# Kernel optimization log

Measured on AMD Instinct MI355X. Metric: run time of the kernel, lower is better.

The kernel has to match this reference:

```python
import jax, jax.numpy as jnp
import numpy as np

N = 50000          # nodes
E = 800000         # edges (before self-loops)
IN = 128           # in_dim
HID = 128          # hidden_dim
HEADS = 4
G = 256            # graphs in batch
EPS = 1e-5         # batchnorm eps
NEG_SLOPE = 0.2    # GATConv leaky_relu slope


def _gat_layer(x, src, dst, W, a_src, a_dst, bias, H, C, concat):
    """PyG-style GATConv (self-loops already appended to src/dst)."""
    n = x.shape[0]
    h = (x @ W).reshape(n, H, C)                       # [N,H,C]
    s_src = (h * a_src).sum(-1)                        # [N,H]
    s_dst = (h * a_dst).sum(-1)                        # [N,H]
    e = jax.nn.leaky_relu(s_src[src] + s_dst[dst], NEG_SLOPE)   # [E',H]
    m = jax.ops.segment_max(e, dst, num_segments=n)    # segment-wise softmax
    ex = jnp.exp(e - m[dst])
    den = jax.ops.segment_sum(ex, dst, num_segments=n)
    alpha = ex / den[dst]                              # [E',H]
    out = jax.ops.segment_sum(alpha[..., None] * h[src], dst, num_segments=n)  # [N,H,C]
    out = out.reshape(n, H * C) if concat else out.mean(axis=1)
    return out + bias


def _bn(x, gamma, beta):
    # PyG BatchNorm over nodes (training-mode batch statistics)
    mu = x.mean(axis=0)
    var = x.var(axis=0)
    return gamma * (x - mu) * jax.lax.rsqrt(var + EPS) + beta


def setup_inputs() -> dict:
    key = jax.random.key(0)
    ks = jax.random.split(key, 32)
    d = {}
    d["x"] = jax.random.normal(ks[0], (N, IN), dtype=jnp.float32)
    d["edge_index"] = jax.random.randint(ks[1], (2, E), 0, N, dtype=jnp.int64)
    d["batch_idx"] = jnp.sort(jax.random.randint(ks[2], (N,), 0, G, dtype=jnp.int64))
    dims = [(IN, HEADS, HID, True), (HID * HEADS, HEADS, HID, True), (HID * HEADS, 1, HID, False)]
    for i, (din, H, C, concat) in enumerate(dims):
        d[f"W{i}"] = jax.random.normal(ks[3 + 4 * i], (din, H * C), dtype=jnp.float32) * 0.05
        d[f"att_src{i}"] = jax.random.normal(ks[4 + 4 * i], (H, C), dtype=jnp.float32) * 0.05
        d[f"att_dst{i}"] = jax.random.normal(ks[5 + 4 * i], (H, C), dtype=jnp.float32) * 0.05
        out_w = H * C if concat else C
        d[f"bias{i}"] = jnp.zeros((out_w,), dtype=jnp.float32)
        d[f"gamma{i}"] = jnp.ones((out_w,), dtype=jnp.float32)
        d[f"beta{i}"] = jnp.zeros((out_w,), dtype=jnp.float32)
    return d


def reference(x, edge_index, batch_idx,
              W0, att_src0, att_dst0, bias0, gamma0, beta0,
              W1, att_src1, att_dst1, bias1, gamma1, beta1,
              W2, att_src2, att_dst2, bias2, gamma2, beta2):
    n = x.shape[0]
    loops = jnp.arange(n, dtype=edge_index.dtype)
    src = jnp.concatenate([edge_index[0], loops])
    dst = jnp.concatenate([edge_index[1], loops])
    layers = [
        (W0, att_src0, att_dst0, bias0, gamma0, beta0, HEADS, HID, True),
        (W1, att_src1, att_dst1, bias1, gamma1, beta1, HEADS, HID, True),
        (W2, att_src2, att_dst2, bias2, gamma2, beta2, 1, HID, False),
    ]
    h = x
    for (W, a_s, a_d, b, g, bt, H, C, concat) in layers:
        h = _gat_layer(h, src, dst, W, a_s, a_d, b, H, C, concat)
        h = jax.nn.elu(_bn(h, g, bt))
        # dropout: identity in eval mode
    # global_mean_pool over batch_idx
    sums = jax.ops.segment_sum(h, batch_idx, num_segments=G)
    cnt = jax.ops.segment_sum(jnp.ones((n,), dtype=h.dtype), batch_idx, num_segments=G)
    return sums / jnp.maximum(cnt, 1.0)[:, None]
```

## Files before the change

### kernel.cpp

```cpp
#include <hip/hip_runtime.h>
#include <math.h>
#include <stdint.h>

#define N_NODES 50000
#define N_EDGES 800000
#define EP      (N_EDGES + N_NODES)
#define G_GRAPHS 256
#define BN_EPS   1e-5f
#define NEG_SLOPE 0.2f

typedef short short8 __attribute__((ext_vector_type(8)));
typedef float f32x4 __attribute__((ext_vector_type(4)));
typedef unsigned short u16;

static __device__ __forceinline__ float lrelu(float x) {
    return x > 0.f ? x : NEG_SLOPE * x;
}

static __device__ __forceinline__ u16 bf16hi(float f) {
    unsigned u = __float_as_uint(f);
    u += 0x7FFFu + ((u >> 16) & 1u);
    return (u16)(u >> 16);
}
static __device__ __forceinline__ float bf2f(u16 h) {
    return __uint_as_float((unsigned)h << 16);
}

static __device__ __forceinline__ void gld_lds16(const void* g, void* l) {
    __builtin_amdgcn_global_load_lds((const __attribute__((address_space(1))) void*)g,
                                     (__attribute__((address_space(3))) void*)l, 16, 0, 0);
}

static __device__ __forceinline__ float2 h2f2(unsigned u) {
    union { unsigned u; _Float16 h[2]; } c;
    c.u = u;
    return make_float2((float)c.h[0], (float)c.h[1]);
}

__global__ void k_hist(const int* __restrict__ ei, int* __restrict__ deg) {
    int stride = gridDim.x * blockDim.x;
    for (int e = blockIdx.x * blockDim.x + threadIdx.x; e < EP; e += stride) {
        int d = (e < N_EDGES) ? ei[N_EDGES + e] : (e - N_EDGES);
        atomicAdd(&deg[d], 1);
    }
}

__global__ void k_scan1(const int* __restrict__ deg, int* __restrict__ row_start,
                        int* __restrict__ totals) {
    __shared__ int buf[1024];
    int t = threadIdx.x;
    int i = blockIdx.x * 1024 + t;
    int v = (i < N_NODES) ? deg[i] : 0;
    buf[t] = v;
    __syncthreads();
    for (int off = 1; off < 1024; off <<= 1) {
        int add = (t >= off) ? buf[t - off] : 0;
        __syncthreads();
        buf[t] += add;
        __syncthreads();
    }
    if (i < N_NODES) row_start[i] = buf[t] - v;
    if (t == 1023) totals[blockIdx.x] = buf[t];
}

__global__ void k_scan2(int* __restrict__ totals, int nb) {
    if (threadIdx.x == 0 && blockIdx.x == 0) {
        int run = 0;
        for (int i = 0; i < nb; ++i) { int v = totals[i]; totals[i] = run; run += v; }
    }
}

__global__ void k_scan3(int* __restrict__ row_start, const int* __restrict__ totals) {
    int i = blockIdx.x * blockDim.x + threadIdx.x;
    if (i < N_NODES) row_start[i] += totals[i >> 10];
    if (i == 0) row_start[N_NODES] = EP;
}

__global__ void k_scatter(const int* __restrict__ ei, const int* __restrict__ row_start,
                          int* __restrict__ cursor, int* __restrict__ csr_src) {
    int stride = gridDim.x * blockDim.x;
    for (int e = blockIdx.x * blockDim.x + threadIdx.x; e < EP; e += stride) {
        int s, d;
        if (e < N_EDGES) { s = ei[e]; d = ei[N_EDGES + e]; }
        else             { s = d = e - N_EDGES; }
        int pos = row_start[d] + atomicAdd(&cursor[d], 1);
        csr_src[pos] = s;
    }
}

__global__ void k_cvtW(const float* __restrict__ W, u16* __restrict__ bthi,
                       u16* __restrict__ btlo, int Nc, int nsh, int KS) {
    int i = blockIdx.x * 256 + threadIdx.x;
    if (i >= (KS << 5) * Nc) return;
    int k = i >> nsh;
    int n = i & (Nc - 1);
    int c = n >> 7, col = n & 127;
    int ks = k >> 5, kq = (k >> 3) & 3, j = k & 7;
    size_t idx = ((size_t)(c * KS + ks)) * 4096 + kq * 1024 + col * 8 + j;
    float v = W[i];
    u16 h = bf16hi(v);
    bthi[idx] = h;
    btlo[idx] = bf16hi(v - bf2f(h));
}

__global__ void k_bnprep(const float* __restrict__ bnsum, const float* __restrict__ bnsq,
                         const float* __restrict__ gamma, const float* __restrict__ beta,
                         float* __restrict__ scale, float* __restrict__ shift, int W) {
    int f = blockIdx.x * 256 + threadIdx.x;
    if (f >= W) return;
    const float invN = 1.f / (float)N_NODES;
    float mean = bnsum[f] * invN;
    float var  = bnsq[f] * invN - mean * mean;
    float sc = gamma[f] * rsqrtf(var + BN_EPS);
    scale[f] = sc;
    shift[f] = beta[f] - mean * sc;
}

template<int AMODE>
__launch_bounds__(256)
__global__ void k_gemm_mfma(const void* __restrict__ Av, const u16* __restrict__ bthi,
                            const u16* __restrict__ btlo, _Float16* __restrict__ C2,
                            float* __restrict__ sSg, float* __restrict__ sDg,
                            const float* __restrict__ asr, const float* __restrict__ adr,
                            const float* __restrict__ scale, const float* __restrict__ shift,
                            int M, int K, int Nc) {
    __shared__ u16 Ah[4096], Al[4096], Bh[4096], Bl[4096];
    __shared__ float rS[128], rD[128];
    const int t    = threadIdx.x;
    const int lane = t & 63, wv = t >> 6;
    const int wr = wv >> 1, wc = wv & 1;
    const int lr = lane & 15, kq = lane >> 4;
    const int r0 = blockIdx.x * 128, c0 = blockIdx.y * 128;
    const int KS = K >> 5;
    const int H = Nc >> 7;
    const int head = blockIdx.y;

    const int ar = t >> 1;
    const int ahf = t & 1;
    const int garow = r0 + ar;
    const bool avalid = garow < M;
    const float*    arowF = (const float*)Av + (size_t)garow * K + ahf * 16;
    const _Float16* arowH = (const _Float16*)Av + (size_t)garow * K + ahf * 16;

    const size_t bchunk0 = (size_t)blockIdx.y * KS * 4096;

    f32x4 acc[4][4];
    #pragma unroll
    for (int m = 0; m < 4; ++m)
        #pragma unroll
        for (int n = 0; n < 4; ++n) {
            acc[m][n][0] = 0.f; acc[m][n][1] = 0.f;
            acc[m][n][2] = 0.f; acc[m][n][3] = 0.f;
        }

    for (int ks = 0; ks < KS; ++ks) {
        float f[16];
        float4 av[4];
        uint4 u0, u1;
        if constexpr (AMODE == 0) {
            const float4* ap = (const float4*)(arowF + ks * 32);
            if (avalid) { av[0] = ap[0]; av[1] = ap[1]; av[2] = ap[2]; av[3] = ap[3]; }
            else av[0] = av[1] = av[2] = av[3] = make_float4(0.f, 0.f, 0.f, 0.f);
        } else {
            if (avalid) {
                u0 = *(const uint4*)(arowH + ks * 32);
                u1 = *(const uint4*)(arowH + ks * 32 + 8);
            } else {
                u0.x = u0.y = u0.z = u0.w = 0u;
                u1.x = u1.y = u1.z = u1.w = 0u;
            }
        }
        __syncthreads();

        if constexpr (AMODE == 0) {
            f[0]=av[0].x; f[1]=av[0].y; f[2]=av[0].z; f[3]=av[0].w;
            f[4]=av[1].x; f[5]=av[1].y; f[6]=av[1].z; f[7]=av[1].w;
            f[8]=av[2].x; f[9]=av[2].y; f[10]=av[2].z; f[11]=av[2].w;
            f[12]=av[3].x; f[13]=av[3].y; f[14]=av[3].z; f[15]=av[3].w;
        } else {
            float2 p0 = h2f2(u0.x), p1 = h2f2(u0.y), p2 = h2f2(u0.z), p3 = h2f2(u0.w);
            float2 p4 = h2f2(u1.x), p5 = h2f2(u1.y), p6 = h2f2(u1.z), p7 = h2f2(u1.w);
            f[0]=p0.x; f[1]=p0.y; f[2]=p1.x; f[3]=p1.y;
            f[4]=p2.x; f[5]=p2.y; f[6]=p3.x; f[7]=p3.y;
            f[8]=p4.x; f[9]=p4.y; f[10]=p5.x; f[11]=p5.y;
            f[12]=p6.x; f[13]=p6.y; f[14]=p7.x; f[15]=p7.y;
            const float* scp = scale + ks * 32 + ahf * 16;
            const float* shp = shift + ks * 32 + ahf * 16;
            #pragma unroll
            for (int i = 0; i < 4; ++i) {
                float4 sc = *(const float4*)(scp + 4 * i);
                float4 sh = *(const float4*)(shp + 4 * i);
                float y;
                y = fmaf(f[4*i+0], sc.x, sh.x); f[4*i+0] = y > 0.f ? y : expm1f(y);
                y = fmaf(f[4*i+1], sc.y, sh.y); f[4*i+1] = y > 0.f ? y : expm1f(y);
                y = fmaf(f[4*i+2], sc.z, sh.z); f[4*i+2] = y > 0.f ? y : expm1f(y);
                y = fmaf(f[4*i+3], sc.w, sh.w); f[4*i+3] = y > 0.f ? y : expm1f(y);
            }
        }

        u16 hi[16], lo[16];
        #pragma unroll
        for (int i = 0; i < 16; ++i) {
            hi[i] = bf16hi(f[i]);
            lo[i] = bf16hi(f[i] - bf2f(hi[i]));
        }
        #pragma unroll
        for (int q = 0; q < 2; ++q) {
            int kqi = ahf * 2 + q;
            int off = kqi * 1024 + ar * 8;
            int4 wh, wl;
            wh.x = (unsigned)hi[q*8+0] | ((unsigned)hi[q*8+1] << 16);
            wh.y = (unsigned)hi[q*8+2] | ((unsigned)hi[q*8+3] << 16);
            wh.z = (unsigned)hi[q*8+4] | ((unsigned)hi[q*8+5] << 16);
            wh.w = (unsigned)hi[q*8+6] | ((unsigned)hi[q*8+7] << 16);
            wl.x = (unsigned)lo[q*8+0] | ((unsigned)lo[q*8+1] << 16);
            wl.y = (unsigned)lo[q*8+2] | ((unsigned)lo[q*8+3] << 16);
            wl.z = (unsigned)lo[q*8+4] | ((unsigned)lo[q*8+5] << 16);
            wl.w = (unsigned)lo[q*8+6] | ((unsigned)lo[q*8+7] << 16);
            *(int4*)&Ah[off] = wh;
            *(int4*)&Al[off] = wl;
        }

        const u16* bhs = bthi + bchunk0 + (size_t)ks * 4096;
        const u16* bls = btlo + bchunk0 + (size_t)ks * 4096;
        #pragma unroll
        for (int p = 0; p < 2; ++p) {
            int ge = p * 2048 + wv * 512 + lane * 8;
            int le = p * 2048 + wv * 512;
            gld_lds16(bhs + ge, &Bh[le]);
            gld_lds16(bls + ge, &Bl[le]);
        }
        __syncthreads();

        short8 afh[4], afl[4], bfh[4], bfl[4];
        #pragma unroll
        for (int m = 0; m < 4; ++m) {
            int row = wr * 64 + m * 16 + lr;
            int off = kq * 1024 + row * 8;
            afh[m] = *(const short8*)&Ah[off];
            afl[m] = *(const short8*)&Al[off];
        }
        #pragma unroll
        for (int n = 0; n < 4; ++n) {
            int col = wc * 64 + n * 16 + lr;
            int off = kq * 1024 + col * 8;
            bfh[n] = *(const short8*)&Bh[off];
            bfl[n] = *(const short8*)&Bl[off];
        }
        #pragma unroll
        for (int m = 0; m < 4; ++m)
            #pragma unroll
            for (int n = 0; n < 4; ++n) {
                acc[m][n] = __builtin_amdgcn_mfma_f32_16x16x32_bf16(afh[m], bfh[n], acc[m][n], 0, 0, 0);
                acc[m][n] = __builtin_amdgcn_mfma_f32_16x16x32_bf16(afh[m], bfl[n], acc[m][n], 0, 0, 0);
                acc[m][n] = __builtin_amdgcn_mfma_f32_16x16x32_bf16(afl[m], bfh[n], acc[m][n], 0, 0, 0);
            }
    }

    float aS[4], aD[4];
    #pragma unroll
    for (int n = 0; n < 4; ++n) {
        int c = c0 + wc * 64 + n * 16 + lr;
        aS[n] = asr[c];
        aD[n] = adr[c];
    }
    __syncthreads();
    if (t < 128) { rS[t] = 0.f; rD[t] = 0.f; }
    __syncthreads();
    #pragma unroll
    for (int m = 0; m < 4; ++m) {
        #pragma unroll
        for (int j = 0; j < 4; ++j) {
            float ps = 0.f, pd = 0.f;
            #pragma unroll
            for (int n = 0; n < 4; ++n) {
                float v = acc[m][n][j];
                ps += v * aS[n];
                pd += v * aD[n];
            }
            #pragma unroll
            for (int off = 1; off < 16; off <<= 1) {
                ps += __shfl_xor(ps, off, 64);
                pd += __shfl_xor(pd, off, 64);
            }
            if (lr == 0) {
                int row = wr * 64 + m * 16 + kq * 4 + j;
                atomicAdd(&rS[row], ps);
                atomicAdd(&rD[row], pd);
            }
        }
    }
    __syncthreads();
    if (t < 128) {
        int r = r0 + t;
        if (r < M) {
            sSg[(size_t)r * H + head] = rS[t];
            sDg[(size_t)r * H + head] = rD[t];
        }
    }

    #pragma unroll
    for (int m = 0; m < 4; ++m) {
        int rowb = r0 + wr * 64 + m * 16 + kq * 4;
        #pragma unroll
        for (int n = 0; n < 4; ++n) {
            int col = c0 + wc * 64 + n * 16 + lr;
            #pragma unroll
            for (int j = 0; j < 4; ++j) {
                int r = rowb + j;
                if (r < M) C2[(size_t)r * Nc + col] = (_Float16)acc[m][n][j];
            }
        }
    }
}

template<int H>
__global__ void k_attn(const float* __restrict__ s_src, const float* __restrict__ s_dst,
                       const int* __restrict__ row_start, const int* __restrict__ csr,
                       float* __restrict__ alpha) {
    int n = blockIdx.x;
    int lane = threadIdx.x;
    const int EPI = 64 / H;
    int head = lane % H;
    int eo   = lane / H;
    int lo = row_start[n], hi = row_start[n + 1];
    float sd = s_dst[n * H + head];
    float* al = alpha + (size_t)head * EP;

    float mx = -INFINITY;
    for (int p = lo + eo; p < hi; p += EPI) {
        int s = csr[p];
        float e = lrelu(s_src[s * H + head] + sd);
        al[p] = e;
        mx = fmaxf(mx, e);
    }
    #pragma unroll
    for (int off = H; off < 64; off <<= 1) mx = fmaxf(mx, __shfl_xor(mx, off, 64));

    float sum = 0.f;
    for (int p = lo + eo; p < hi; p += EPI) {
        float ex = expf(al[p] - mx);
        al[p] = ex;
        sum += ex;
    }
    #pragma unroll
    for (int off = H; off < 64; off <<= 1) sum += __shfl_xor(sum, off, 64);

    float inv = 1.f / sum;
    for (int p = lo + eo; p < hi; p += EPI) al[p] *= inv;
}

template<int H, int CPT>
__global__ void k_agg2(const _Float16* __restrict__ hb2, const float* __restrict__ alpha,
                       const int* __restrict__ row_start, const int* __restrict__ csr,
                       const float* __restrict__ bias, _Float16* __restrict__ out) {
    const int W = H * 128;
    int n = blockIdx.x;
    int t = threadIdx.x;
    int c0 = t * CPT;
    int head = c0 >> 7;
    const float* al = alpha + (size_t)head * EP;
    int lo = row_start[n], hi = row_start[n + 1];
    float acc[CPT];
    #pragma unroll
    for (int j = 0; j < CPT; ++j) acc[j] = 0.f;

    int p = lo;
    for (; p + 4 <= hi; p += 4) {
        int s0 = csr[p], s1 = csr[p+1], s2 = csr[p+2], s3 = csr[p+3];
        float l0 = al[p], l1 = al[p+1], l2 = al[p+2], l3 = al[p+3];
        if constexpr (CPT == 4) {
            uint2 v0 = *(const uint2*)&hb2[(size_t)s0 * W + c0];
            uint2 v1 = *(const uint2*)&hb2[(size_t)s1 * W + c0];
            uint2 v2 = *(const uint2*)&hb2[(size_t)s2 * W + c0];
            uint2 v3 = *(const uint2*)&hb2[(size_t)s3 * W + c0];
            float2 a, b;
            a = h2f2(v0.x); b = h2f2(v0.y);
            acc[0] += l0*a.x; acc[1] += l0*a.y; acc[2] += l0*b.x; acc[3] += l0*b.y;
            a = h2f2(v1.x); b = h2f2(v1.y);
            acc[0] += l1*a.x; acc[1] += l1*a.y; acc[2] += l1*b.x; acc[3] += l1*b.y;
            a = h2f2(v2.x); b = h2f2(v2.y);
            acc[0] += l2*a.x; acc[1] += l2*a.y; acc[2] += l2*b.x; acc[3] += l2*b.y;
            a = h2f2(v3.x); b = h2f2(v3.y);
            acc[0] += l3*a.x; acc[1] += l3*a.y; acc[2] += l3*b.x; acc[3] += l3*b.y;
        } else {
            unsigned v0 = *(const unsigned*)&hb2[(size_t)s0 * W + c0];
            unsigned v1 = *(const unsigned*)&hb2[(size_t)s1 * W + c0];
            unsigned v2 = *(const unsigned*)&hb2[(size_t)s2 * W + c0];
            unsigned v3 = *(const unsigned*)&hb2[(size_t)s3 * W + c0];
            float2 a;
            a = h2f2(v0); acc[0] += l0*a.x; acc[1] += l0*a.y;
            a = h2f2(v1); acc[0] += l1*a.x; acc[1] += l1*a.y;
            a = h2f2(v2); acc[0] += l2*a.x; acc[1] += l2*a.y;
            a = h2f2(v3); acc[0] += l3*a.x; acc[1] += l3*a.y;
        }
    }
    for (; p < hi; ++p) {
        int s0 = csr[p];
        float l0 = al[p];
        if constexpr (CPT == 4) {
            uint2 v0 = *(const uint2*)&hb2[(size_t)s0 * W + c0];
            float2 a = h2f2(v0.x), b = h2f2(v0.y);
            acc[0] += l0*a.x; acc[1] += l0*a.y; acc[2] += l0*b.x; acc[3] += l0*b.y;
        } else {
            float2 a = h2f2(*(const unsigned*)&hb2[(size_t)s0 * W + c0]);
            acc[0] += l0*a.x; acc[1] += l0*a.y;
        }
    }

    union { _Float16 h[CPT]; unsigned u[CPT/2]; } pk;
    #pragma unroll
    for (int j = 0; j < CPT; ++j) pk.h[j] = (_Float16)(acc[j] + bias[c0 + j]);
    if constexpr (CPT == 4)
        *(uint2*)&out[(size_t)n * W + c0] = *(uint2*)pk.u;
    else
        *(unsigned*)&out[(size_t)n * W + c0] = pk.u[0];
}

__global__ void k_bnstat2(const _Float16* __restrict__ x, float* __restrict__ bnsum,
                          float* __restrict__ bnsq, int W) {
    const int RPB = 64;
    int t  = threadIdx.x;
    int r0 = blockIdx.x * RPB;
    int r1 = min(r0 + RPB, N_NODES);
    float s0 = 0.f, q0 = 0.f, s1 = 0.f, q1 = 0.f;
    for (int r = r0; r < r1; ++r) {
        float2 v = h2f2(*(const unsigned*)&x[(size_t)r * W + 2 * t]);
        s0 += v.x; q0 += v.x * v.x;
        s1 += v.y; q1 += v.y * v.y;
    }
    atomicAdd(&bnsum[2*t],   s0);
    atomicAdd(&bnsq[2*t],    q0);
    atomicAdd(&bnsum[2*t+1], s1);
    atomicAdd(&bnsq[2*t+1],  q1);
}

__global__ void k_pool(const _Float16* __restrict__ x, const int* __restrict__ batch,
                       const float* __restrict__ scale, const float* __restrict__ shift,
                       float* __restrict__ out) {
    int g = blockIdx.x;
    int f = threadIdx.x;
    int a = 0, b = N_NODES;
    while (a < b) { int m = (a + b) >> 1; if (batch[m] < g) a = m + 1; else b = m; }
    int lo = a;
    b = N_NODES;
    while (a < b) { int m = (a + b) >> 1; if (batch[m] < g + 1) a = m + 1; else b = m; }
    int hi = a;
    float sc = scale[f], sh = shift[f];
    float s = 0.f;
    for (int r = lo; r < hi; ++r) {
        float v = (float)x[(size_t)r * 128 + f];
        float y = fmaf(v, sc, sh);
        s += (y > 0.f) ? y : expm1f(y);
    }
    int cnt = hi - lo;
    out[g * 128 + f] = s / (float)(cnt > 0 ? cnt : 1);
}

extern "C" void kernel_launch(void* const* d_in, const int* in_sizes, int n_in,
                              void* d_out, int out_size, void* d_ws, size_t ws_size,
                              hipStream_t stream) {
    const float* x     = (const float*)d_in[0];
    const int*   ei    = (const int*)d_in[1];
    const int*   batch = (const int*)d_in[2];
    const float* Wm[3]  = {(const float*)d_in[3],  (const float*)d_in[9],  (const float*)d_in[15]};
    const float* asr[3] = {(const float*)d_in[4],  (const float*)d_in[10], (const float*)d_in[16]};
    const float* adr[3] = {(const float*)d_in[5],  (const float*)d_in[11], (const float*)d_in[17]};
    const float* bia[3] = {(const float*)d_in[6],  (const float*)d_in[12], (const float*)d_in[18]};
    const float* gam[3] = {(const float*)d_in[7],  (const float*)d_in[13], (const float*)d_in[19]};
    const float* bet[3] = {(const float*)d_in[8],  (const float*)d_in[14], (const float*)d_in[20]};

    char* w = (char*)d_ws;
    auto alloc = [&](size_t bytes) -> void* {
        void* p = (void*)w;
        w += (bytes + 255) & ~(size_t)255;
        return p;
    };
    _Float16* act2   = (_Float16*)alloc((size_t)N_NODES * 512 * 2);
    _Float16* act128 = (_Float16*)alloc((size_t)N_NODES * 128 * 2);
    _Float16* hb2    = (_Float16*)alloc((size_t)N_NODES * 512 * 2);
    float*   alpha = (float*)alloc((size_t)EP * 4 * 4);
    int* csr_src   = (int*)alloc((size_t)EP * 4);
    int* row_start = (int*)alloc((size_t)(N_NODES + 1) * 4);
    int* deg       = (int*)alloc((size_t)N_NODES * 4);
    int* cursor    = (int*)alloc((size_t)N_NODES * 4);
    float* s_src = (float*)alloc((size_t)N_NODES * 4 * 4);
    float* s_dst = (float*)alloc((size_t)N_NODES * 4 * 4);
    float* bn    = (float*)alloc(1024 * 4);
    float* scl   = (float*)alloc(512 * 4);
    float* shf   = (float*)alloc(512 * 4);
    int* totals  = (int*)alloc(64 * 4);
    u16* bthi = (u16*)alloc((size_t)512 * 512 * 2);
    u16* btlo = (u16*)alloc((size_t)512 * 512 * 2);

    hipMemsetAsync(deg, 0, (size_t)N_NODES * 4, stream);
    hipMemsetAsync(cursor, 0, (size_t)N_NODES * 4, stream);
    k_hist<<<512, 256, 0, stream>>>(ei, deg);
    k_scan1<<<(N_NODES + 1023) / 1024, 1024, 0, stream>>>(deg, row_start, totals);
    k_scan2<<<1, 64, 0, stream>>>(totals, (N_NODES + 1023) / 1024);
    k_scan3<<<(N_NODES + 255) / 256, 256, 0, stream>>>(row_start, totals);
    k_scatter<<<512, 256, 0, stream>>>(ei, row_start, cursor, csr_src);

    auto layer = [&](const void* Ain, int K, int li, int H, int amode, _Float16* outAct) {
        int Wd = H * 128;
        int nsh = (Wd == 512) ? 9 : 7;
        int tot = K * Wd;
        k_cvtW<<<(tot + 255) / 256, 256, 0, stream>>>(Wm[li], bthi, btlo, Wd, nsh, K >> 5);
        dim3 gg((N_NODES + 127) / 128, Wd / 128);
        if (amode == 0)
            k_gemm_mfma<0><<<gg, 256, 0, stream>>>(Ain, bthi, btlo, hb2, s_src, s_dst,
                                                   asr[li], adr[li], scl, shf, N_NODES, K, Wd);
        else
            k_gemm_mfma<1><<<gg, 256, 0, stream>>>(Ain, bthi, btlo, hb2, s_src, s_dst,
                                                   asr[li], adr[li], scl, shf, N_NODES, K, Wd);
        if (H == 4) {
            k_attn<4><<<N_NODES, 64, 0, stream>>>(s_src, s_dst, row_start, csr_src, alpha);
            k_agg2<4, 4><<<N_NODES, 128, 0, stream>>>(hb2, alpha, row_start, csr_src, bia[li], outAct);
        } else {
            k_attn<1><<<N_NODES, 64, 0, stream>>>(s_src, s_dst, row_start, csr_src, alpha);
            k_agg2<1, 2><<<N_NODES, 64, 0, stream>>>(hb2, alpha, row_start, csr_src, bia[li], outAct);
        }
        hipMemsetAsync(bn, 0, 1024 * 4, stream);
        k_bnstat2<<<(N_NODES + 63) / 64, Wd / 2, 0, stream>>>(outAct, bn, bn + 512, Wd);
        k_bnprep<<<(Wd + 255) / 256, 256, 0, stream>>>(bn, bn + 512, gam[li], bet[li], scl, shf, Wd);
    };

    layer(x,    128, 0, 4, 0, act2);
    layer(act2, 512, 1, 4, 1, act2);
    layer(act2, 512, 2, 1, 1, act128);

    k_pool<<<G_GRAPHS, 128, 0, stream>>>(act128, batch, scl, shf, (float*)d_out);
}
```

Before: 973.0 us.

## Switch GEMM to fp16 MFMA with pre-swizzled fp16 A operand

Replaces the three-pass bf16 split GEMM with a two-pass fp16 scheme: A is rounded once to fp16 and B keeps a hi/lo fp16 split. A separate prep kernel applies BN+ELU, converts A to fp16 and writes it in the MFMA-friendly swizzled layout, so the GEMM loads A straight to LDS. This removes one MFMA pass per tile and the per-K-step conversion work inside the GEMM. The cost is an extra kernel pass over A per layer, with its global write and reread, and less precision on A because it is no longer split into hi/lo parts.

```diff
diff --git a/kernel.cpp b/kernel.cpp
--- a/kernel.cpp
+++ b/kernel.cpp
@@ -3,27 +3,18 @@
 #include <stdint.h>
 
 #define N_NODES 50000
+#define NPAD    50048
 #define N_EDGES 800000
 #define EP      (N_EDGES + N_NODES)
 #define G_GRAPHS 256
 #define BN_EPS   1e-5f
 #define NEG_SLOPE 0.2f
 
-typedef short short8 __attribute__((ext_vector_type(8)));
 typedef float f32x4 __attribute__((ext_vector_type(4)));
-typedef unsigned short u16;
+typedef _Float16 h16x8 __attribute__((ext_vector_type(8)));
 
 static __device__ __forceinline__ float lrelu(float x) {
     return x > 0.f ? x : NEG_SLOPE * x;
-}
-
-static __device__ __forceinline__ u16 bf16hi(float f) {
-    unsigned u = __float_as_uint(f);
-    u += 0x7FFFu + ((u >> 16) & 1u);
-    return (u16)(u >> 16);
-}
-static __device__ __forceinline__ float bf2f(u16 h) {
-    return __uint_as_float((unsigned)h << 16);
 }
 
 static __device__ __forceinline__ void gld_lds16(const void* g, void* l) {
@@ -88,19 +79,19 @@
     }
 }
 
-__global__ void k_cvtW(const float* __restrict__ W, u16* __restrict__ bthi,
-                       u16* __restrict__ btlo, int Nc, int nsh, int KS) {
+__global__ void k_cvtW(const float* __restrict__ W, _Float16* __restrict__ bthi,
+                       _Float16* __restrict__ btlo, int Nc, int nsh, int KS) {
     int i = blockIdx.x * 256 + threadIdx.x;
     if (i >= (KS << 5) * Nc) return;
     int k = i >> nsh;
     int n = i & (Nc - 1);
     int c = n >> 7, col = n & 127;
     int ks = k >> 5, kq = (k >> 3) & 3, j = k & 7;
-    size_t idx = ((size_t)(c * KS + ks)) * 4096 + kq * 1024 + col * 8 + j;
+    size_t idx = ((size_t)(c * KS + ks) << 12) + (kq << 10) + (col << 3) + j;
     float v = W[i];
-    u16 h = bf16hi(v);
+    _Float16 h = (_Float16)v;
     bthi[idx] = h;
-    btlo[idx] = bf16hi(v - bf2f(h));
+    btlo[idx] = (_Float16)(v - (float)h);
 }
 
 __global__ void k_bnprep(const float* __restrict__ bnsum, const float* __restrict__ bnsq,
@@ -116,15 +107,69 @@
     shift[f] = beta[f] - mean * sc;
 }
 
-template<int AMODE>
+__global__ void k_prepA0(const float* __restrict__ x, _Float16* __restrict__ Aswz,
+                         int K, int s8, int KS) {
+    int i = blockIdx.x * 256 + threadIdx.x;
+    if (i >= NPAD * (K >> 3)) return;
+    int r  = i >> s8;
+    int c8 = i & ((K >> 3) - 1);
+    int k  = c8 << 3;
+    union { _Float16 h[8]; uint4 u; } pk;
+    if (r < N_NODES) {
+        float4 a0 = *(const float4*)&x[(size_t)r * K + k];
+        float4 a1 = *(const float4*)&x[(size_t)r * K + k + 4];
+        pk.h[0]=(_Float16)a0.x; pk.h[1]=(_Float16)a0.y; pk.h[2]=(_Float16)a0.z; pk.h[3]=(_Float16)a0.w;
+        pk.h[4]=(_Float16)a1.x; pk.h[5]=(_Float16)a1.y; pk.h[6]=(_Float16)a1.z; pk.h[7]=(_Float16)a1.w;
+    } else {
+        pk.u.x = pk.u.y = pk.u.z = pk.u.w = 0u;
+    }
+    int rb = r >> 7, row = r & 127;
+    int ks = k >> 5, kq = (k >> 3) & 3;
+    size_t idx = ((size_t)(rb * KS + ks) << 12) + (kq << 10) + (row << 3);
+    *(uint4*)&Aswz[idx] = pk.u;
+}
+
+__global__ void k_prepA1(const _Float16* __restrict__ act, const float* __restrict__ scale,
+                         const float* __restrict__ shift, _Float16* __restrict__ Aswz,
+                         int K, int s8, int KS) {
+    int i = blockIdx.x * 256 + threadIdx.x;
+    if (i >= NPAD * (K >> 3)) return;
+    int r  = i >> s8;
+    int c8 = i & ((K >> 3) - 1);
+    int k  = c8 << 3;
+    union { _Float16 h[8]; uint4 u; } pk;
+    if (r < N_NODES) {
+        uint4 v = *(const uint4*)&act[(size_t)r * K + k];
+        float4 sc0 = *(const float4*)&scale[k];
+        float4 sc1 = *(const float4*)&scale[k + 4];
+        float4 sh0 = *(const float4*)&shift[k];
+        float4 sh1 = *(const float4*)&shift[k + 4];
+        float2 p0 = h2f2(v.x), p1 = h2f2(v.y), p2 = h2f2(v.z), p3 = h2f2(v.w);
+        float y;
+        y = fmaf(p0.x, sc0.x, sh0.x); pk.h[0] = (_Float16)(y > 0.f ? y : expm1f(y));
+        y = fmaf(p0.y, sc0.y, sh0.y); pk.h[1] = (_Float16)(y > 0.f ? y : expm1f(y));
+        y = fmaf(p1.x, sc0.z, sh0.z); pk.h[2] = (_Float16)(y > 0.f ? y : expm1f(y));
+        y = fmaf(p1.y, sc0.w, sh0.w); pk.h[3] = (_Float16)(y > 0.f ? y : expm1f(y));
+        y = fmaf(p2.x, sc1.x, sh1.x); pk.h[4] = (_Float16)(y > 0.f ? y : expm1f(y));
+        y = fmaf(p2.y, sc1.y, sh1.y); pk.h[5] = (_Float16)(y > 0.f ? y : expm1f(y));
+        y = fmaf(p3.x, sc1.z, sh1.z); pk.h[6] = (_Float16)(y > 0.f ? y : expm1f(y));
+        y = fmaf(p3.y, sc1.w, sh1.w); pk.h[7] = (_Float16)(y > 0.f ? y : expm1f(y));
+    } else {
+        pk.u.x = pk.u.y = pk.u.z = pk.u.w = 0u;
+    }
+    int rb = r >> 7, row = r & 127;
+    int ks = k >> 5, kq = (k >> 3) & 3;
+    size_t idx = ((size_t)(rb * KS + ks) << 12) + (kq << 10) + (row << 3);
+    *(uint4*)&Aswz[idx] = pk.u;
+}
+
 __launch_bounds__(256)
-__global__ void k_gemm_mfma(const void* __restrict__ Av, const u16* __restrict__ bthi,
-                            const u16* __restrict__ btlo, _Float16* __restrict__ C2,
-                            float* __restrict__ sSg, float* __restrict__ sDg,
-                            const float* __restrict__ asr, const float* __restrict__ adr,
-                            const float* __restrict__ scale, const float* __restrict__ shift,
-                            int M, int K, int Nc) {
-    __shared__ u16 Ah[4096], Al[4096], Bh[4096], Bl[4096];
+__global__ void k_gemm_f16(const _Float16* __restrict__ Aswz, const _Float16* __restrict__ bthi,
+                           const _Float16* __restrict__ btlo, _Float16* __restrict__ C2,
+                           float* __restrict__ sSg, float* __restrict__ sDg,
+                           const float* __restrict__ asr, const float* __restrict__ adr,
+                           int M, int K, int Nc) {
+    __shared__ _Float16 Ah[4096], Bh[4096], Bl[4096];
     __shared__ float rS[128], rD[128];
     const int t    = threadIdx.x;
     const int lane = t & 63, wv = t >> 6;
@@ -135,13 +180,7 @@
     const int H = Nc >> 7;
     const int head = blockIdx.y;
 
-    const int ar = t >> 1;
-    const int ahf = t & 1;
-    const int garow = r0 + ar;
-    const bool avalid = garow < M;
-    const float*    arowF = (const float*)Av + (size_t)garow * K + ahf * 16;
-    const _Float16* arowH = (const _Float16*)Av + (size_t)garow * K + ahf * 16;
-
+    const size_t achunk0 = (size_t)blockIdx.x * KS * 4096;
     const size_t bchunk0 = (size_t)blockIdx.y * KS * 4096;
 
     f32x4 acc[4][4];
@@ -154,106 +193,38 @@
         }
 
     for (int ks = 0; ks < KS; ++ks) {
-        float f[16];
-        float4 av[4];
-        uint4 u0, u1;
-        if constexpr (AMODE == 0) {
-            const float4* ap = (const float4*)(arowF + ks * 32);
-            if (avalid) { av[0] = ap[0]; av[1] = ap[1]; av[2] = ap[2]; av[3] = ap[3]; }
-            else av[0] = av[1] = av[2] = av[3] = make_float4(0.f, 0.f, 0.f, 0.f);
-        } else {
-            if (avalid) {
-                u0 = *(const uint4*)(arowH + ks * 32);
-                u1 = *(const uint4*)(arowH + ks * 32 + 8);
-            } else {
-                u0.x = u0.y = u0.z = u0.w = 0u;
-                u1.x = u1.y = u1.z = u1.w = 0u;
-            }
-        }
         __syncthreads();
-
-        if constexpr (AMODE == 0) {
-            f[0]=av[0].x; f[1]=av[0].y; f[2]=av[0].z; f[3]=av[0].w;
-            f[4]=av[1].x; f[5]=av[1].y; f[6]=av[1].z; f[7]=av[1].w;
-            f[8]=av[2].x; f[9]=av[2].y; f[10]=av[2].z; f[11]=av[2].w;
-            f[12]=av[3].x; f[13]=av[3].y; f[14]=av[3].z; f[15]=av[3].w;
-        } else {
-            float2 p0 = h2f2(u0.x), p1 = h2f2(u0.y), p2 = h2f2(u0.z), p3 = h2f2(u0.w);
-            float2 p4 = h2f2(u1.x), p5 = h2f2(u1.y), p6 = h2f2(u1.z), p7 = h2f2(u1.w);
-            f[0]=p0.x; f[1]=p0.y; f[2]=p1.x; f[3]=p1.y;
-            f[4]=p2.x; f[5]=p2.y; f[6]=p3.x; f[7]=p3.y;
-            f[8]=p4.x; f[9]=p4.y; f[10]=p5.x; f[11]=p5.y;
-            f[12]=p6.x; f[13]=p6.y; f[14]=p7.x; f[15]=p7.y;
-            const float* scp = scale + ks * 32 + ahf * 16;
-            const float* shp = shift + ks * 32 + ahf * 16;
-            #pragma unroll
-            for (int i = 0; i < 4; ++i) {
-                float4 sc = *(const float4*)(scp + 4 * i);
-                float4 sh = *(const float4*)(shp + 4 * i);
-                float y;
-                y = fmaf(f[4*i+0], sc.x, sh.x); f[4*i+0] = y > 0.f ? y : expm1f(y);
-                y = fmaf(f[4*i+1], sc.y, sh.y); f[4*i+1] = y > 0.f ? y : expm1f(y);
-                y = fmaf(f[4*i+2], sc.z, sh.z); f[4*i+2] = y > 0.f ? y : expm1f(y);
-                y = fmaf(f[4*i+3], sc.w, sh.w); f[4*i+3] = y > 0.f ? y : expm1f(y);
-            }
-        }
-
-        u16 hi[16], lo[16];
-        #pragma unroll
-        for (int i = 0; i < 16; ++i) {
-            hi[i] = bf16hi(f[i]);
-            lo[i] = bf16hi(f[i] - bf2f(hi[i]));
-        }
-        #pragma unroll
-        for (int q = 0; q < 2; ++q) {
-            int kqi = ahf * 2 + q;
-            int off = kqi * 1024 + ar * 8;
-            int4 wh, wl;
-            wh.x = (unsigned)hi[q*8+0] | ((unsigned)hi[q*8+1] << 16);
-            wh.y = (unsigned)hi[q*8+2] | ((unsigned)hi[q*8+3] << 16);
-            wh.z = (unsigned)hi[q*8+4] | ((unsigned)hi[q*8+5] << 16);
-            wh.w = (unsigned)hi[q*8+6] | ((unsigned)hi[q*8+7] << 16);
-            wl.x = (unsigned)lo[q*8+0] | ((unsigned)lo[q*8+1] << 16);
-            wl.y = (unsigned)lo[q*8+2] | ((unsigned)lo[q*8+3] << 16);
-            wl.z = (unsigned)lo[q*8+4] | ((unsigned)lo[q*8+5] << 16);
-            wl.w = (unsigned)lo[q*8+6] | ((unsigned)lo[q*8+7] << 16);
-            *(int4*)&Ah[off] = wh;
-            *(int4*)&Al[off] = wl;
-        }
-
-        const u16* bhs = bthi + bchunk0 + (size_t)ks * 4096;
-        const u16* bls = btlo + bchunk0 + (size_t)ks * 4096;
+        const _Float16* as  = Aswz + achunk0 + ((size_t)ks << 12);
+        const _Float16* bhs = bthi + bchunk0 + ((size_t)ks << 12);
+        const _Float16* bls = btlo + bchunk0 + ((size_t)ks << 12);
         #pragma unroll
         for (int p = 0; p < 2; ++p) {
             int ge = p * 2048 + wv * 512 + lane * 8;
             int le = p * 2048 + wv * 512;
+            gld_lds16(as  + ge, &Ah[le]);
             gld_lds16(bhs + ge, &Bh[le]);
             gld_lds16(bls + ge, &Bl[le]);
         }
         __syncthreads();
 
-        short8 afh[4], afl[4], bfh[4], bfl[4];
+        h16x8 af[4], bfh[4], bfl[4];
         #pragma unroll
         for (int m = 0; m < 4; ++m) {
             int row = wr * 64 + m * 16 + lr;
-            int off = kq * 1024 + row * 8;
-            afh[m] = *(const short8*)&Ah[off];
-            afl[m] = *(const short8*)&Al[off];
+            af[m] = *(const h16x8*)&Ah[kq * 1024 + row * 8];
         }
         #pragma unroll
         for (int n = 0; n < 4; ++n) {
             int col = wc * 64 + n * 16 + lr;
-            int off = kq * 1024 + col * 8;
-            bfh[n] = *(const short8*)&Bh[off];
-            bfl[n] = *(const short8*)&Bl[off];
+            bfh[n] = *(const h16x8*)&Bh[kq * 1024 + col * 8];
+            bfl[n] = *(const h16x8*)&Bl[kq * 1024 + col * 8];
         }
         #pragma unroll
         for (int m = 0; m < 4; ++m)
             #pragma unroll
             for (int n = 0; n < 4; ++n) {
-                acc[m][n] = __builtin_amdgcn_mfma_f32_16x16x32_bf16(afh[m], bfh[n], acc[m][n], 0, 0, 0);
-                acc[m][n] = __builtin_amdgcn_mfma_f32_16x16x32_bf16(afh[m], bfl[n], acc[m][n], 0, 0, 0);
-                acc[m][n] = __builtin_amdgcn_mfma_f32_16x16x32_bf16(afl[m], bfh[n], acc[m][n], 0, 0, 0);
+                acc[m][n] = __builtin_amdgcn_mfma_f32_16x16x32_f16(af[m], bfh[n], acc[m][n], 0, 0, 0);
+                acc[m][n] = __builtin_amdgcn_mfma_f32_16x16x32_f16(af[m], bfl[n], acc[m][n], 0, 0, 0);
             }
     }
 
@@ -479,6 +450,7 @@
     _Float16* act2   = (_Float16*)alloc((size_t)N_NODES * 512 * 2);
     _Float16* act128 = (_Float16*)alloc((size_t)N_NODES * 128 * 2);
     _Float16* hb2    = (_Float16*)alloc((size_t)N_NODES * 512 * 2);
+    _Float16* Aswz   = (_Float16*)alloc((size_t)NPAD * 512 * 2);
     float*   alpha = (float*)alloc((size_t)EP * 4 * 4);
     int* csr_src   = (int*)alloc((size_t)EP * 4);
     int* row_start = (int*)alloc((size_t)(N_NODES + 1) * 4);
@@ -490,8 +462,8 @@
     float* scl   = (float*)alloc(512 * 4);
     float* shf   = (float*)alloc(512 * 4);
     int* totals  = (int*)alloc(64 * 4);
-    u16* bthi = (u16*)alloc((size_t)512 * 512 * 2);
-    u16* btlo = (u16*)alloc((size_t)512 * 512 * 2);
+    _Float16* bthi = (_Float16*)alloc((size_t)512 * 512 * 2);
+    _Float16* btlo = (_Float16*)alloc((size_t)512 * 512 * 2);
 
     hipMemsetAsync(deg, 0, (size_t)N_NODES * 4, stream);
     hipMemsetAsync(cursor, 0, (size_t)N_NODES * 4, stream);
@@ -501,18 +473,21 @@
     k_scan3<<<(N_NODES + 255) / 256, 256, 0, stream>>>(row_start, totals);
     k_scatter<<<512, 256, 0, stream>>>(ei, row_start, cursor, csr_src);
 
-    auto layer = [&](const void* Ain, int K, int li, int H, int amode, _Float16* outAct) {
+    auto layer = [&](int K, int li, int H, bool first, _Float16* outAct) {
         int Wd = H * 128;
         int nsh = (Wd == 512) ? 9 : 7;
+        int KS = K >> 5;
+        int s8 = (K == 512) ? 6 : 4;
         int tot = K * Wd;
-        k_cvtW<<<(tot + 255) / 256, 256, 0, stream>>>(Wm[li], bthi, btlo, Wd, nsh, K >> 5);
-        dim3 gg((N_NODES + 127) / 128, Wd / 128);
-        if (amode == 0)
-            k_gemm_mfma<0><<<gg, 256, 0, stream>>>(Ain, bthi, btlo, hb2, s_src, s_dst,
-                                                   asr[li], adr[li], scl, shf, N_NODES, K, Wd);
+        k_cvtW<<<(tot + 255) / 256, 256, 0, stream>>>(Wm[li], bthi, btlo, Wd, nsh, KS);
+        int ptot = NPAD * (K >> 3);
+        if (first)
+            k_prepA0<<<(ptot + 255) / 256, 256, 0, stream>>>(x, Aswz, K, s8, KS);
         else
-            k_gemm_mfma<1><<<gg, 256, 0, stream>>>(Ain, bthi, btlo, hb2, s_src, s_dst,
-                                                   asr[li], adr[li], scl, shf, N_NODES, K, Wd);
+            k_prepA1<<<(ptot + 255) / 256, 256, 0, stream>>>(act2, scl, shf, Aswz, K, s8, KS);
+        dim3 gg(NPAD / 128, Wd / 128);
+        k_gemm_f16<<<gg, 256, 0, stream>>>(Aswz, bthi, btlo, hb2, s_src, s_dst,
+                                           asr[li], adr[li], N_NODES, K, Wd);
         if (H == 4) {
             k_attn<4><<<N_NODES, 64, 0, stream>>>(s_src, s_dst, row_start, csr_src, alpha);
             k_agg2<4, 4><<<N_NODES, 128, 0, stream>>>(hb2, alpha, row_start, csr_src, bia[li], outAct);
@@ -525,9 +500,9 @@
         k_bnprep<<<(Wd + 255) / 256, 256, 0, stream>>>(bn, bn + 512, gam[li], bet[li], scl, shf, Wd);
     };
 
-    layer(x,    128, 0, 4, 0, act2);
-    layer(act2, 512, 1, 4, 1, act2);
-    layer(act2, 512, 2, 1, 1, act128);
+    layer(128, 0, 4, true,  act2);
+    layer(512, 1, 4, false, act2);
+    layer(512, 2, 1, false, act128);
 
     k_pool<<<G_GRAPHS, 128, 0, stream>>>(act128, batch, scl, shf, (float*)d_out);
 }
```

Measured after the change: 924.3 us. 5.0% less time.
